# Kernel tuning notes

Measured on AMD Instinct MI355X. Metric: run time of the kernel, lower is better.

## Reference

```python
import jax, jax.numpy as jnp
import numpy as np
import math

B, SEQ_IN, D_IN = 4, 1028, 64
D = 1024          # hidden_size
H = 16            # num_heads
HD = D // H       # head_dim
L = 4             # num_layers
D_OUT = 1
EPS = 1e-6


def setup_inputs() -> dict:
    key = jax.random.key(0)
    ks = iter(jax.random.split(key, 32))
    s = 0.02
    inp = {}
    inp['x'] = jax.random.normal(next(ks), (B, SEQ_IN, D_IN), jnp.float32)
    # conv frontend (torch Conv1d weight layout: [out_ch, in_ch, k])
    inp['conv1_w'] = jax.random.normal(next(ks), (D // 2, D_IN, 3), jnp.float32) * s
    inp['conv1_b'] = jnp.zeros((D // 2,), jnp.float32)
    inp['conv2_w'] = jax.random.normal(next(ks), (D, D // 2, 3), jnp.float32) * s
    inp['conv2_b'] = jnp.zeros((D,), jnp.float32)
    # stacked per-layer params [L, ...]
    inp['lnA_w'] = jnp.ones((L, D), jnp.float32)
    inp['lnA_b'] = jnp.zeros((L, D), jnp.float32)
    inp['q_w'] = jax.random.normal(next(ks), (L, D, D), jnp.float32) * s
    inp['q_b'] = jnp.zeros((L, D), jnp.float32)
    inp['k_w'] = jax.random.normal(next(ks), (L, D, D), jnp.float32) * s
    inp['k_b'] = jnp.zeros((L, D), jnp.float32)
    inp['v_w'] = jax.random.normal(next(ks), (L, D, D), jnp.float32) * s
    inp['v_b'] = jnp.zeros((L, D), jnp.float32)
    inp['o_w'] = jax.random.normal(next(ks), (L, D, D), jnp.float32) * s
    inp['o_b'] = jnp.zeros((L, D), jnp.float32)
    inp['lnB_w'] = jnp.ones((L, D), jnp.float32)
    inp['lnB_b'] = jnp.zeros((L, D), jnp.float32)
    inp['f1_w'] = jax.random.normal(next(ks), (L, 2 * D, D), jnp.float32) * s
    inp['f1_b'] = jnp.zeros((L, 2 * D), jnp.float32)
    inp['f2_w'] = jax.random.normal(next(ks), (L, D, 2 * D), jnp.float32) * s
    inp['f2_b'] = jnp.zeros((L, D), jnp.float32)
    inp['fc_w'] = jax.random.normal(next(ks), (D_OUT, D), jnp.float32) * s
    inp['fc_b'] = jnp.zeros((D_OUT,), jnp.float32)
    return inp


def _layernorm(x, w, b):
    # torch-style: unbiased std (ddof=1), eps added to std (not var)
    mean = jnp.mean(x, axis=-1, keepdims=True)
    var = jnp.sum((x - mean) ** 2, axis=-1, keepdims=True) / (x.shape[-1] - 1)
    return w * ((x - mean) / (jnp.sqrt(var) + EPS)) + b


def _pos_encoding(S, d):
    pos = jnp.arange(S, dtype=jnp.float32)[:, None]
    div = jnp.exp(jnp.arange(0, d, 2, dtype=jnp.float32) * (-math.log(10000.0) / d))
    pe = jnp.zeros((S, d), jnp.float32)
    pe = pe.at[:, 0::2].set(jnp.sin(pos * div))
    pe = pe.at[:, 1::2].set(jnp.cos(pos * div))
    return pe


def _forward(x, conv1_w, conv1_b, conv2_w, conv2_b,
             lnA_w, lnA_b, q_w, q_b, k_w, k_b, v_w, v_b, o_w, o_b,
             lnB_w, lnB_b, f1_w, f1_b, f2_w, f2_b, fc_w, fc_b):
    dn = ('NCH', 'OIH', 'NCH')
    h = jnp.transpose(x, (0, 2, 1))                       # [B, D_in, S_in]
    h = jax.lax.conv_general_dilated(h, conv1_w, (1,), 'VALID', dimension_numbers=dn) + conv1_b[None, :, None]
    h = jax.lax.conv_general_dilated(h, conv2_w, (1,), 'VALID', dimension_numbers=dn) + conv2_b[None, :, None]
    h = jnp.transpose(h, (0, 2, 1))                       # [B, S, D]
    S = h.shape[1]
    h = h + _pos_encoding(S, D)[None]
    scale = 1.0 / math.sqrt(HD)

    def layer(xc, p):
        (lnaw, lnab, qw, qb, kw, kb, vw, vb, ow, ob,
         lnbw, lnbb, f1w, f1b, f2w, f2b) = p
        hn = _layernorm(xc, lnaw, lnab)
        q = (hn @ qw.T + qb).reshape(B, S, H, HD).transpose(0, 2, 1, 3)
        k = (hn @ kw.T + kb).reshape(B, S, H, HD).transpose(0, 2, 1, 3)
        v = (hn @ vw.T + vb).reshape(B, S, H, HD).transpose(0, 2, 1, 3)
        scores = jnp.einsum('bhsd,bhtd->bhst', q, k) * scale
        attn = scores / (1.0 + jnp.abs(scores))           # softsign, NOT softmax
        wv = jnp.einsum('bhst,bhtd->bhsd', attn, v)
        wv = wv.transpose(0, 2, 1, 3).reshape(B, S, D)
        xc = xc + (wv @ ow.T + ob)
        hn2 = _layernorm(xc, lnbw, lnbb)
        ff = jax.nn.relu(hn2 @ f1w.T + f1b) @ f2w.T + f2b
        return xc + ff, None

    params = (lnA_w, lnA_b, q_w, q_b, k_w, k_b, v_w, v_b, o_w, o_b,
              lnB_w, lnB_b, f1_w, f1_b, f2_w, f2_b)
    h, _ = jax.lax.scan(layer, h, params)
    pooled = jnp.mean(h, axis=1)                          # [B, D]
    return pooled @ fc_w.T + fc_b                         # [B, D_OUT]


def reference(x, conv1_w, conv1_b, conv2_w, conv2_b,
              lnA_w, lnA_b, q_w, q_b, k_w, k_b, v_w, v_b, o_w, o_b,
              lnB_w, lnB_b, f1_w, f1_b, f2_w, f2_b, fc_w, fc_b):
    return _forward(x, conv1_w, conv1_b, conv2_w, conv2_b,
                    lnA_w, lnA_b, q_w, q_b, k_w, k_b, v_w, v_b, o_w, o_b,
                    lnB_w, lnB_b, f1_w, f1_b, f2_w, f2_b, fc_w, fc_b)
```

## Files before the change

kernel.cpp:

```cpp
#include <hip/hip_runtime.h>
#include <hip/hip_bf16.h>
#include <math.h>

typedef __bf16 v8bf __attribute__((ext_vector_type(8)));
typedef float  v4f  __attribute__((ext_vector_type(4)));
typedef unsigned short v8us __attribute__((ext_vector_type(8)));

__device__ __forceinline__ unsigned short f2bfu(float f) {
    unsigned u = __builtin_bit_cast(unsigned, f);
    unsigned r = (u + 0x7fffu + ((u >> 16) & 1u)) >> 16;
    return (unsigned short)r;
}
__device__ __forceinline__ float bf2f(unsigned short u) {
    unsigned x = ((unsigned)u) << 16;
    return __builtin_bit_cast(float, x);
}

__device__ __forceinline__ long long swidx(int r, int k, int kt ) {
    return ((long long)((r >> 4) * kt + (k >> 5)) << 9)
         + (((k >> 3) & 3) << 7) + ((r & 15) << 3) + (k & 7);
}

#define GLDS16(g, s)                                                        \
    __builtin_amdgcn_global_load_lds(                                       \
        (const __attribute__((address_space(1))) void*)(g),                 \
        (__attribute__((address_space(3))) void*)(s), 16, 0, 0)

#define LOAD_CHUNK(R, C) do {                                               \
    const long long o_ = (long long)(C) << 9;                               \
    _Pragma("unroll")                                                       \
    for (int i_ = 0; i_ < 4; i_++) Ab[R][i_] = *(const v8bf*)(pa[i_] + o_); \
    _Pragma("unroll")                                                       \
    for (int j_ = 0; j_ < 4; j_++) Bb[R][j_] = *(const v8bf*)(pb[j_] + o_); \
} while (0)

#define MFMA_CHUNK(R) do {                                                  \
    _Pragma("unroll")                                                       \
    for (int i_ = 0; i_ < 4; i_++)                                          \
    _Pragma("unroll")                                                       \
    for (int j_ = 0; j_ < 4; j_++)                                          \
        acc[i_][j_] = __builtin_amdgcn_mfma_f32_16x16x32_bf16(              \
            Ab[R][i_], Bb[R][j_], acc[i_][j_], 0, 0, 0);                    \
} while (0)

__global__ __launch_bounds__(64, 2) void gemm_sw_k(
    const unsigned short* __restrict__ Asw,
    const unsigned short* __restrict__ Bsw,
    const float* __restrict__ bias,
    const float* __restrict__ res,
    float* __restrict__ Cf,
    unsigned short* __restrict__ Cb,
    unsigned short* __restrict__ Csw,
    unsigned short* __restrict__ Ct, int ctcol0,
    int M, int N, int K, int ldC, int relu)
{
    const int l = threadIdx.x;

    int bx = blockIdx.x, by = blockIdx.y;
    {
        int nbx = gridDim.x, nby = gridDim.y;
        if (((nbx & 7) == 0) && ((nby & 15) == 0)) {
            int bid   = by * nbx + bx;
            int xcd   = bid & 7;
            int local = bid >> 3;
            int rby = nby >> 2;
            int rbx = nbx >> 1;
            int u   = local & 15;
            int mt  = local >> 4;
            int mtxc = rbx >> 2;
            int mty = mt / mtxc;
            int mtx = mt - mty * mtxc;
            by = (xcd >> 1) * rby + (mty << 2) + (u >> 2);
            bx = (xcd & 1) * rbx + (mtx << 2) + (u & 3);
        } else {
            int nb = nbx * nby;
            if ((nb & 7) == 0) {
                int bid = by * nbx + bx;
                int nid = (bid & 7) * (nb >> 3) + (bid >> 3);
                by = nid / nbx;
                bx = nid - by * nbx;
            }
        }
    }
    const int m0 = by * 64;
    const int n0 = bx * 64;
    const int r16 = l & 15;
    const int qb  = l >> 4;
    const int kt = K >> 5;

    const unsigned short* pa[4];
#pragma unroll
    for (int i = 0; i < 4; i++)
        pa[i] = Asw + ((long long)(((m0 >> 4) + i) * kt) << 9) + l * 8;
    const unsigned short* pb[4];
#pragma unroll
    for (int j = 0; j < 4; j++)
        pb[j] = Bsw + ((long long)(((n0 >> 4) + j) * kt) << 9) + l * 8;

    v4f acc[4][4];
#pragma unroll
    for (int i = 0; i < 4; i++)
#pragma unroll
        for (int j = 0; j < 4; j++) acc[i][j] = (v4f){0.f, 0.f, 0.f, 0.f};

    v8bf Ab[4][4], Bb[4][4];

    LOAD_CHUNK(0, 0);
    LOAD_CHUNK(1, 1);
    LOAD_CHUNK(2, 2);

    int s = 0;
    for (; s < kt - 4; s += 4) {
        LOAD_CHUNK(3, s + 3); MFMA_CHUNK(0);
        LOAD_CHUNK(0, s + 4); MFMA_CHUNK(1);
        LOAD_CHUNK(1, s + 5); MFMA_CHUNK(2);
        LOAD_CHUNK(2, s + 6); MFMA_CHUNK(3);
    }
    LOAD_CHUNK(3, kt - 1);
    MFMA_CHUNK(0); MFMA_CHUNK(1); MFMA_CHUNK(2); MFMA_CHUNK(3);

    float bv[4];
#pragma unroll
    for (int j = 0; j < 4; j++) bv[j] = bias[n0 + 16 * j + r16];
    const int colbase = n0 + r16;
    const int nt = N >> 5;
#pragma unroll
    for (int i = 0; i < 4; i++) {
        int rowb = m0 + 16 * i + qb * 4;
#pragma unroll
        for (int j = 0; j < 4; j++) {
            int col = colbase + 16 * j;
            float v[4];
#pragma unroll
            for (int r = 0; r < 4; r++) v[r] = acc[i][j][r] + bv[j];
            if (Ct && col >= ctcol0) {
                ushort4 o;
                o.x = f2bfu(v[0]); o.y = f2bfu(v[1]);
                o.z = f2bfu(v[2]); o.w = f2bfu(v[3]);
                *(ushort4*)(Ct + ((long long)(rowb >> 10) << 20)
                            + (long long)(col - ctcol0) * 1024 + (rowb & 1023)) = o;
            } else if (Csw) {
#pragma unroll
                for (int r = 0; r < 4; r++) {
                    int row = rowb + r;
                    float vv = v[r];
                    if (relu) vv = fmaxf(vv, 0.f);
                    Csw[swidx(row, col, nt)] = f2bfu(vv);
                }
            } else {
#pragma unroll
                for (int r = 0; r < 4; r++) {
                    int row = rowb + r;
                    long long off = (long long)row * ldC + col;
                    float vv = v[r];
                    if (res)  vv += res[off];
                    if (relu) vv = fmaxf(vv, 0.f);
                    if (Cf) Cf[off] = vv;
                    if (Cb) ((unsigned short*)Cb)[off] = f2bfu(vv);
                }
            }
        }
    }
}

__global__ __launch_bounds__(256) void gemm_mfma_k(
    const __hip_bfloat16* __restrict__ A, int rpbA, long long bstrideA, int ldA,
    const __hip_bfloat16* __restrict__ B,
    const float* __restrict__ bias,
    const float* __restrict__ res,
    float* __restrict__ Cf,
    __hip_bfloat16* __restrict__ Cb,
    int M, int N, int K, int ldC, int relu)
{
    __shared__ __align__(16) __hip_bfloat16 As[2][8][64][8];
    __shared__ __align__(16) __hip_bfloat16 Bs[2][4][64][8];
    const int t  = threadIdx.x;
    const int w  = t >> 6;
    const int l  = t & 63;
    const int m0 = blockIdx.y * 128;
    const int n0 = blockIdx.x * 64;
    const int r16 = l & 15;
    const int qb  = l >> 4;
    const int wm = w >> 1, wn = w & 1;

    const __hip_bfloat16* gA[2];
#pragma unroll
    for (int tt = 0; tt < 2; tt++) {
        int arow = m0 + 16 * (2 * w + tt) + r16;
        gA[tt] = A + (long long)(arow / rpbA) * bstrideA
                   + (long long)(arow % rpbA) * ldA + qb * 8;
    }
    const __hip_bfloat16* gB = B + (long long)(n0 + 16 * w + r16) * K + qb * 8;

    v4f acc[4][2];
#pragma unroll
    for (int i = 0; i < 4; i++)
#pragma unroll
        for (int j = 0; j < 2; j++) acc[i][j] = (v4f){0.f, 0.f, 0.f, 0.f};

    GLDS16(gA[0], &As[0][2 * w + 0][0][0]);
    GLDS16(gA[1], &As[0][2 * w + 1][0][0]);
    GLDS16(gB,    &Bs[0][w][0][0]);
    __syncthreads();

    int cur = 0;
    for (int k0 = 32; k0 < K; k0 += 32) {
        v8bf af[4], bfr[2];
#pragma unroll
        for (int i = 0; i < 4; i++) af[i]  = *(const v8bf*)(&As[cur][4 * wm + i][l][0]);
#pragma unroll
        for (int j = 0; j < 2; j++) bfr[j] = *(const v8bf*)(&Bs[cur][2 * wn + j][l][0]);
        GLDS16(gA[0] + k0, &As[cur ^ 1][2 * w + 0][0][0]);
        GLDS16(gA[1] + k0, &As[cur ^ 1][2 * w + 1][0][0]);
        GLDS16(gB + k0,    &Bs[cur ^ 1][w][0][0]);
#pragma unroll
        for (int i = 0; i < 4; i++)
#pragma unroll
            for (int j = 0; j < 2; j++)
                acc[i][j] = __builtin_amdgcn_mfma_f32_16x16x32_bf16(
                    af[i], bfr[j], acc[i][j], 0, 0, 0);
        __syncthreads();
        cur ^= 1;
    }
    {
        v8bf af[4], bfr[2];
#pragma unroll
        for (int i = 0; i < 4; i++) af[i]  = *(const v8bf*)(&As[cur][4 * wm + i][l][0]);
#pragma unroll
        for (int j = 0; j < 2; j++) bfr[j] = *(const v8bf*)(&Bs[cur][2 * wn + j][l][0]);
#pragma unroll
        for (int i = 0; i < 4; i++)
#pragma unroll
            for (int j = 0; j < 2; j++)
                acc[i][j] = __builtin_amdgcn_mfma_f32_16x16x32_bf16(
                    af[i], bfr[j], acc[i][j], 0, 0, 0);
    }

    float bv[2];
#pragma unroll
    for (int j = 0; j < 2; j++) bv[j] = bias[n0 + 32 * wn + 16 * j + r16];
    const int colbase = n0 + 32 * wn + r16;
#pragma unroll
    for (int i = 0; i < 4; i++) {
        int rowb = m0 + 64 * wm + 16 * i + qb * 4;
#pragma unroll
        for (int j = 0; j < 2; j++) {
            int col = colbase + 16 * j;
#pragma unroll
            for (int r = 0; r < 4; r++) {
                int row = rowb + r;
                if (row >= M) continue;
                long long off = (long long)row * ldC + col;
                float vv = acc[i][j][r] + bv[j];
                if (res)  vv += res[off];
                if (relu) vv = fmaxf(vv, 0.f);
                if (Cf) Cf[off] = vv;
                if (Cb) ((unsigned short*)Cb)[off] = f2bfu(vv);
            }
        }
    }
}

__global__ __launch_bounds__(256) void attn_mfma_k(
    const unsigned short* __restrict__ QKV,
    const unsigned short* __restrict__ Vt,
    unsigned short* __restrict__ Osw)
{
    __shared__ __align__(16) unsigned short lds[25600];
    const int t = threadIdx.x, w = t >> 6, l = t & 63;
    const int bh = blockIdx.y, b = bh >> 4, h = bh & 15;
    const int s0 = blockIdx.x << 7;
    const int r16 = l & 15, q4 = l >> 4;
    const long long qrow0 = (long long)(b << 10) + s0;
    const int hoff = h << 6;

#pragma unroll
    for (int mi = 0; mi < 2; mi++)
#pragma unroll
        for (int kk = 0; kk < 2; kk++) {
            const unsigned short* g = QKV + (qrow0 + 32 * w + 16 * mi + r16) * 3072
                                      + hoff + 32 * kk + q4 * 8;
            GLDS16(g, &lds[(w * 4 + mi * 2 + kk) * 512]);
        }
    __syncthreads();
    v8bf qf[2][2];
#pragma unroll
    for (int mi = 0; mi < 2; mi++)
#pragma unroll
        for (int kk = 0; kk < 2; kk++)
            qf[mi][kk] = *(const v8bf*)&lds[(w * 4 + mi * 2 + kk) * 512 + l * 8];

    v4f oacc[2][4];
#pragma unroll
    for (int i = 0; i < 2; i++)
#pragma unroll
        for (int j = 0; j < 4; j++) oacc[i][j] = (v4f){0.f, 0.f, 0.f, 0.f};

    for (int t0 = 0; t0 < 1024; t0 += 64) {
#pragma unroll
        for (int rr = 0; rr < 2; rr++) {
            int r = 2 * w + rr, kk = r >> 2, j = r & 3;
            const unsigned short* gk = QKV
                + ((long long)(b << 10) + t0 + 16 * j + r16) * 3072
                + 1024 + hoff + 32 * kk + q4 * 8;
            GLDS16(gk, &lds[8192 + r * 512]);
            const unsigned short* gv = Vt + ((long long)b << 20)
                + (long long)(hoff + 16 * j + r16) * 1024 + t0 + 32 * kk + q4 * 8;
            GLDS16(gv, &lds[12288 + r * 512]);
        }
        __syncthreads();

        v8bf kf[2][4];
#pragma unroll
        for (int kk = 0; kk < 2; kk++)
#pragma unroll
            for (int j = 0; j < 4; j++)
                kf[kk][j] = *(const v8bf*)&lds[8192 + (kk * 4 + j) * 512 + l * 8];
        v4f sc[2][4];
#pragma unroll
        for (int i = 0; i < 2; i++)
#pragma unroll
            for (int j = 0; j < 4; j++) sc[i][j] = (v4f){0.f, 0.f, 0.f, 0.f};
#pragma unroll
        for (int kk = 0; kk < 2; kk++)
#pragma unroll
            for (int mi = 0; mi < 2; mi++)
#pragma unroll
                for (int j = 0; j < 4; j++)
                    sc[mi][j] = __builtin_amdgcn_mfma_f32_16x16x32_bf16(
                        qf[mi][kk], kf[kk][j], sc[mi][j], 0, 0, 0);

#pragma unroll
        for (int mi = 0; mi < 2; mi++)
#pragma unroll
            for (int j = 0; j < 4; j++)
#pragma unroll
                for (int r = 0; r < 4; r++) {
                    float v = sc[mi][j][r] * 0.125f;
                    float p = v * __builtin_amdgcn_rcpf(1.0f + fabsf(v));
                    lds[16384 + (32 * w + 16 * mi + q4 * 4 + r) * 72 + 16 * j + r16] = f2bfu(p);
                }

        v8bf pf[2][2], vf[2][4];
#pragma unroll
        for (int mi = 0; mi < 2; mi++)
#pragma unroll
            for (int kk = 0; kk < 2; kk++)
                pf[mi][kk] = *(const v8bf*)&lds[16384 + (32 * w + 16 * mi + r16) * 72
                                                + 32 * kk + q4 * 8];
#pragma unroll
        for (int kk = 0; kk < 2; kk++)
#pragma unroll
            for (int j = 0; j < 4; j++)
                vf[kk][j] = *(const v8bf*)&lds[12288 + (kk * 4 + j) * 512 + l * 8];
#pragma unroll
        for (int kk = 0; kk < 2; kk++)
#pragma unroll
            for (int mi = 0; mi < 2; mi++)
#pragma unroll
                for (int j = 0; j < 4; j++)
                    oacc[mi][j] = __builtin_amdgcn_mfma_f32_16x16x32_bf16(
                        pf[mi][kk], vf[kk][j], oacc[mi][j], 0, 0, 0);
        __syncthreads();
    }

#pragma unroll
    for (int mi = 0; mi < 2; mi++)
#pragma unroll
        for (int j = 0; j < 4; j++)
#pragma unroll
            for (int r = 0; r < 4; r++)
                lds[(32 * w + 16 * mi + q4 * 4 + r) * 72 + 16 * j + r16] =
                    f2bfu(oacc[mi][j][r]);
    __syncthreads();
    {
        int row = t >> 1, ch = (t & 1) << 5;
        int grow = (int)qrow0 + row;
#pragma unroll
        for (int i = 0; i < 4; i++) {
            int c0 = hoff + ch + 8 * i;
            v8us vv = *(const v8us*)&lds[row * 72 + ch + 8 * i];
            *(v8us*)(Osw + swidx(grow, c0, 32)) = vv;
        }
    }
}

__global__ __launch_bounds__(256) void layernorm_k(
    const float* __restrict__ x, const float* __restrict__ w,
    const float* __restrict__ b, unsigned short* __restrict__ ysw)
{
    int row = blockIdx.x;
    int t = threadIdx.x;
    float4 v = ((const float4*)(x + ((long long)row << 10)))[t];
    float s = v.x + v.y + v.z + v.w;
#pragma unroll
    for (int o = 32; o; o >>= 1) s += __shfl_down(s, o);
    __shared__ float red[4];
    __shared__ float red2[4];
    int wid = t >> 6, lane = t & 63;
    if (lane == 0) red[wid] = s;
    __syncthreads();
    float mean = (red[0] + red[1] + red[2] + red[3]) * (1.0f / 1024.0f);
    float dx = v.x - mean, dy = v.y - mean, dz = v.z - mean, dw = v.w - mean;
    float sq = dx * dx + dy * dy + dz * dz + dw * dw;
#pragma unroll
    for (int o = 32; o; o >>= 1) sq += __shfl_down(sq, o);
    if (lane == 0) red2[wid] = sq;
    __syncthreads();
    float var = (red2[0] + red2[1] + red2[2] + red2[3]) * (1.0f / 1023.0f);
    float inv = 1.0f / (sqrtf(var) + 1e-6f);
    float4 W  = ((const float4*)w)[t];
    float4 Bv = ((const float4*)b)[t];
    ushort4 o;
    o.x = f2bfu(W.x * (dx * inv) + Bv.x);
    o.y = f2bfu(W.y * (dy * inv) + Bv.y);
    o.z = f2bfu(W.z * (dz * inv) + Bv.z);
    o.w = f2bfu(W.w * (dw * inv) + Bv.w);
    int c0 = t << 2;
    *(ushort4*)(ysw + swidx(row, c0, 32)) = o;
}

__global__ __launch_bounds__(256) void add_pos_k(float* __restrict__ h)
{
    int idx = blockIdx.x * 256 + threadIdx.x;
    int d = idx & 1023;
    int s = (idx >> 10) & 1023;
    int e = d & ~1;
    float div = expf(-9.210340371976184f * (float)e * (1.0f / 1024.0f));
    float arg = (float)s * div;
    float pe = (d & 1) ? cosf(arg) : sinf(arg);
    h[idx] += pe;
}

__global__ __launch_bounds__(256) void convert_k(
    const float* __restrict__ src, unsigned short* __restrict__ dst, int n4)
{
    int i = blockIdx.x * 256 + threadIdx.x;
    if (i >= n4) return;
    float4 v = ((const float4*)src)[i];
    ushort4 o;
    o.x = f2bfu(v.x); o.y = f2bfu(v.y); o.z = f2bfu(v.z); o.w = f2bfu(v.w);
    ((ushort4*)dst)[i] = o;
}

__global__ __launch_bounds__(256) void convert_layer_sw_k(
    const float* __restrict__ q, const float* __restrict__ k,
    const float* __restrict__ v, const float* __restrict__ o,
    const float* __restrict__ f1, const float* __restrict__ f2,
    unsigned short* __restrict__ dst)
{
    int idx = blockIdx.x * 256 + threadIdx.x;
    const float* src;
    unsigned short* db;
    int Ksh, rf;
    if (idx < 0x100000) {
        int region = idx >> 18;
        rf = idx & 0x3FFFF;
        src = (region == 0) ? q : (region == 1) ? k : (region == 2) ? v : o;
        db = dst + ((long long)region << 20);
        Ksh = 10;
    } else if (idx < 0x180000) {
        rf = idx - 0x100000; src = f1; db = dst + (4LL << 20); Ksh = 10;
    } else {
        rf = idx - 0x180000; src = f2; db = dst + (6LL << 20); Ksh = 11;
    }
    float4 vv = ((const float4*)src)[rf];
    int flatf = rf << 2;
    int n  = flatf >> Ksh;
    int k0 = flatf & ((1 << Ksh) - 1);
    ushort4 ov;
    ov.x = f2bfu(vv.x); ov.y = f2bfu(vv.y); ov.z = f2bfu(vv.z); ov.w = f2bfu(vv.w);
    *(ushort4*)(db + swidx(n, k0, 1 << (Ksh - 5))) = ov;
}

__global__ __launch_bounds__(256) void concat3_k(
    const float* __restrict__ a, const float* __restrict__ b,
    const float* __restrict__ c, float* __restrict__ o)
{
    int i = blockIdx.x * 256 + threadIdx.x;
    o[i] = (i < 1024) ? a[i] : ((i < 2048) ? b[i - 1024] : c[i - 2048]);
}

__global__ __launch_bounds__(256) void reorder_w_k(
    const float* __restrict__ src, unsigned short* __restrict__ dst, int OC, int IC)
{
    int idx = blockIdx.x * 256 + threadIdx.x;
    if (idx >= OC * IC * 3) return;
    int k  = idx % 3;
    int ic = (idx / 3) % IC;
    int oc = idx / (3 * IC);
    dst[(oc * 3 + k) * IC + ic] = f2bfu(src[idx]);
}

__global__ __launch_bounds__(256) void meanpool_part_k(
    const float* __restrict__ h, float* __restrict__ part)
{
    int g = blockIdx.x;
    int b = g >> 6, rblk = g & 63;
    const float4* base = (const float4*)(h + ((long long)b << 20)
                                           + ((long long)(rblk * 16) << 10));
    float4 s = {0.f, 0.f, 0.f, 0.f};
#pragma unroll
    for (int i = 0; i < 16; i++) {
        float4 v = base[i * 256 + threadIdx.x];
        s.x += v.x; s.y += v.y; s.z += v.z; s.w += v.w;
    }
    ((float4*)part)[g * 256 + threadIdx.x] = s;
}

__global__ __launch_bounds__(256) void meanpool_red_k(
    const float* __restrict__ part, float* __restrict__ pooled)
{
    int idx = blockIdx.x * 256 + threadIdx.x;
    int b = idx >> 10, d = idx & 1023;
    const float* p = part + ((long long)(b * 64) << 10) + d;
    float s = 0.f;
#pragma unroll 8
    for (int r = 0; r < 64; r++) s += p[r << 10];
    pooled[idx] = s * (1.0f / 1024.0f);
}

__global__ __launch_bounds__(256) void fc_k(
    const float* __restrict__ p, const float* __restrict__ w,
    const float* __restrict__ fb, float* __restrict__ out)
{
    int b = blockIdx.x, t = threadIdx.x;
    float s = 0.f;
    for (int i = t; i < 1024; i += 256) s += p[(b << 10) + i] * w[i];
#pragma unroll
    for (int o = 32; o; o >>= 1) s += __shfl_down(s, o);
    __shared__ float red[4];
    if ((t & 63) == 0) red[t >> 6] = s;
    __syncthreads();
    if (t == 0) out[b] = red[0] + red[1] + red[2] + red[3] + fb[0];
}

extern "C" void kernel_launch(void* const* d_in, const int* in_sizes, int n_in,
                              void* d_out, int out_size, void* d_ws, size_t ws_size,
                              hipStream_t stream)
{
    const float* x    = (const float*)d_in[0];
    const float* c1w  = (const float*)d_in[1];
    const float* c1b  = (const float*)d_in[2];
    const float* c2w  = (const float*)d_in[3];
    const float* c2b  = (const float*)d_in[4];
    const float* lnAw = (const float*)d_in[5];
    const float* lnAb = (const float*)d_in[6];
    const float* qw   = (const float*)d_in[7];
    const float* qbi  = (const float*)d_in[8];
    const float* kw   = (const float*)d_in[9];
    const float* kbi  = (const float*)d_in[10];
    const float* vw   = (const float*)d_in[11];
    const float* vbi  = (const float*)d_in[12];
    const float* ow   = (const float*)d_in[13];
    const float* obi  = (const float*)d_in[14];
    const float* lnBw = (const float*)d_in[15];
    const float* lnBb = (const float*)d_in[16];
    const float* f1w  = (const float*)d_in[17];
    const float* f1b  = (const float*)d_in[18];
    const float* f2w  = (const float*)d_in[19];
    const float* f2b  = (const float*)d_in[20];
    const float* fcw  = (const float*)d_in[21];
    const float* fcb  = (const float*)d_in[22];
    float* out = (float*)d_out;

    float* ws = (float*)d_ws;
    typedef __hip_bfloat16 bf;
    typedef unsigned short us;
    float* h    = ws;
    us* hn_b    = (us*)(ws + 4194304);
    us* qkv_b   = (us*)(ws + 6291456);
    us* ff_b    = qkv_b;
    us* wq_b    = (us*)(ws + 12582912);
    us* wo_b    = (us*)(ws + 14155776);
    us* wf1_b   = (us*)(ws + 14680064);
    us* wf2_b   = (us*)(ws + 15728640);
    us* xb      = (us*)(ws + 16777216);
    us* h1b     = (us*)(ws + 16912896);
    us* w1t_b   = (us*)(ws + 17963520);
    us* w2t_b   = (us*)(ws + 18012672);
    float* pooled = ws + 18799104;
    us* Vt      = (us*)(ws + 18803200);
    float* bqkv = ws + 20900352;
    float* mp_part = ws + 20903424;

    convert_k<<<dim3(257), 256, 0, stream>>>(x, xb, 65792);
    reorder_w_k<<<dim3(384),  256, 0, stream>>>(c1w, w1t_b, 512, 64);
    reorder_w_k<<<dim3(6144), 256, 0, stream>>>(c2w, w2t_b, 1024, 512);

    gemm_mfma_k<<<dim3(8, 33), 256, 0, stream>>>(
        (const bf*)xb, 1026, 1028LL * 64, 64, (const bf*)w1t_b,
        c1b, nullptr, nullptr, (bf*)h1b, 4104, 512, 192, 512, 0);
    gemm_mfma_k<<<dim3(16, 32), 256, 0, stream>>>(
        (const bf*)h1b, 1024, 1026LL * 512, 512, (const bf*)w2t_b,
        c2b, nullptr, h, nullptr, 4096, 1024, 1536, 1024, 0);
    add_pos_k<<<dim3(16384), 256, 0, stream>>>(h);

    for (int l = 0; l < 4; l++) {
        long long wo  = (long long)l * 1048576;
        long long wo2 = (long long)l * 2097152;
        convert_layer_sw_k<<<dim3(8192), 256, 0, stream>>>(
            qw + wo, kw + wo, vw + wo, ow + wo, f1w + wo2, f2w + wo2, wq_b);
        concat3_k<<<dim3(12), 256, 0, stream>>>(qbi + l * 1024, kbi + l * 1024,
                                                vbi + l * 1024, bqkv);

        layernorm_k<<<dim3(4096), 256, 0, stream>>>(h, lnAw + l * 1024, lnAb + l * 1024, hn_b);
        gemm_sw_k<<<dim3(48, 64), 64, 0, stream>>>(
            hn_b, wq_b, bqkv, nullptr, nullptr, qkv_b, nullptr, Vt, 2048,
            4096, 3072, 1024, 3072, 0);
        attn_mfma_k<<<dim3(8, 64), 256, 0, stream>>>(qkv_b, Vt, hn_b);
        gemm_sw_k<<<dim3(16, 64), 64, 0, stream>>>(
            hn_b, wo_b, obi + l * 1024, h, h, nullptr, nullptr, nullptr, 0,
            4096, 1024, 1024, 1024, 0);
        layernorm_k<<<dim3(4096), 256, 0, stream>>>(h, lnBw + l * 1024, lnBb + l * 1024, hn_b);
        gemm_sw_k<<<dim3(32, 64), 64, 0, stream>>>(
            hn_b, wf1_b, f1b + l * 2048, nullptr, nullptr, nullptr, ff_b, nullptr, 0,
            4096, 2048, 1024, 2048, 1);
        gemm_sw_k<<<dim3(16, 64), 64, 0, stream>>>(
            ff_b, wf2_b, f2b + l * 1024, h, h, nullptr, nullptr, nullptr, 0,
            4096, 1024, 2048, 1024, 0);
    }

    meanpool_part_k<<<dim3(256), 256, 0, stream>>>(h, mp_part);
    meanpool_red_k<<<dim3(16), 256, 0, stream>>>(mp_part, pooled);
    fc_k<<<dim3(4), 256, 0, stream>>>(pooled, fcw, fcb, out);
}
```

Measured before the change: 1.122 ms.

## Double-buffer K/V tiles in attention and use two-wave GEMM blocks

The attention kernel now prefetches the next 64-key K/V tile into a second LDS buffer while the current tile is processed. This moves the P scratch to the start of LDS and drops the per-iteration load-then-sync stall. The swizzled GEMM switches to 128-thread blocks, each wave computing an adjacent 64-column tile, so grids halve in x and the A rows are shared across two waves. Grid swizzle conditions change with the new grid sizes, and LDS layout offsets must not overlap the P scratch.

```diff
diff --git a/kernel.cpp b/kernel.cpp
--- a/kernel.cpp
+++ b/kernel.cpp
@@ -43,7 +43,7 @@
             Ab[R][i_], Bb[R][j_], acc[i_][j_], 0, 0, 0);                    \
 } while (0)
 
-__global__ __launch_bounds__(64, 2) void gemm_sw_k(
+__global__ __launch_bounds__(128, 2) void gemm_sw_k(
     const unsigned short* __restrict__ Asw,
     const unsigned short* __restrict__ Bsw,
     const float* __restrict__ bias,
@@ -54,7 +54,8 @@
     unsigned short* __restrict__ Ct, int ctcol0,
     int M, int N, int K, int ldC, int relu)
 {
-    const int l = threadIdx.x;
+    const int wv = threadIdx.x >> 6;
+    const int l  = threadIdx.x & 63;
 
     int bx = blockIdx.x, by = blockIdx.y;
     {
@@ -83,7 +84,7 @@
         }
     }
     const int m0 = by * 64;
-    const int n0 = bx * 64;
+    const int n0 = bx * 128 + wv * 64;
     const int r16 = l & 15;
     const int qb  = l >> 4;
     const int kt = K >> 5;
@@ -274,6 +275,21 @@
     const long long qrow0 = (long long)(b << 10) + s0;
     const int hoff = h << 6;
 
+#define LOAD_KV(T0, KVW) do {                                               \
+    _Pragma("unroll")                                                       \
+    for (int rr_ = 0; rr_ < 2; rr_++) {                                     \
+        int r_ = 2 * w + rr_, kk_ = r_ >> 2, j_ = r_ & 3;                   \
+        const unsigned short* gk_ = QKV                                     \
+            + ((long long)(b << 10) + (T0) + 16 * j_ + r16) * 3072          \
+            + 1024 + hoff + 32 * kk_ + q4 * 8;                              \
+        GLDS16(gk_, &lds[(KVW) + r_ * 512]);                                \
+        const unsigned short* gv_ = Vt + ((long long)b << 20)               \
+            + (long long)(hoff + 16 * j_ + r16) * 1024 + (T0)               \
+            + 32 * kk_ + q4 * 8;                                            \
+        GLDS16(gv_, &lds[(KVW) + 4096 + r_ * 512]);                         \
+    }                                                                       \
+} while (0)
+
 #pragma unroll
     for (int mi = 0; mi < 2; mi++)
 #pragma unroll
@@ -282,6 +298,7 @@
                                       + hoff + 32 * kk + q4 * 8;
             GLDS16(g, &lds[(w * 4 + mi * 2 + kk) * 512]);
         }
+    LOAD_KV(0, 9216);
     __syncthreads();
     v8bf qf[2][2];
 #pragma unroll
@@ -289,6 +306,7 @@
 #pragma unroll
         for (int kk = 0; kk < 2; kk++)
             qf[mi][kk] = *(const v8bf*)&lds[(w * 4 + mi * 2 + kk) * 512 + l * 8];
+    __syncthreads();
 
     v4f oacc[2][4];
 #pragma unroll
@@ -296,26 +314,17 @@
 #pragma unroll
         for (int j = 0; j < 4; j++) oacc[i][j] = (v4f){0.f, 0.f, 0.f, 0.f};
 
-    for (int t0 = 0; t0 < 1024; t0 += 64) {
-#pragma unroll
-        for (int rr = 0; rr < 2; rr++) {
-            int r = 2 * w + rr, kk = r >> 2, j = r & 3;
-            const unsigned short* gk = QKV
-                + ((long long)(b << 10) + t0 + 16 * j + r16) * 3072
-                + 1024 + hoff + 32 * kk + q4 * 8;
-            GLDS16(gk, &lds[8192 + r * 512]);
-            const unsigned short* gv = Vt + ((long long)b << 20)
-                + (long long)(hoff + 16 * j + r16) * 1024 + t0 + 32 * kk + q4 * 8;
-            GLDS16(gv, &lds[12288 + r * 512]);
-        }
-        __syncthreads();
+    int cur = 0;
+    for (int it = 0; it < 16; ++it) {
+        const int kvr = 9216 + cur * 8192;
+        if (it < 15) LOAD_KV((it + 1) * 64, 9216 + (cur ^ 1) * 8192);
 
         v8bf kf[2][4];
 #pragma unroll
         for (int kk = 0; kk < 2; kk++)
 #pragma unroll
             for (int j = 0; j < 4; j++)
-                kf[kk][j] = *(const v8bf*)&lds[8192 + (kk * 4 + j) * 512 + l * 8];
+                kf[kk][j] = *(const v8bf*)&lds[kvr + (kk * 4 + j) * 512 + l * 8];
         v4f sc[2][4];
 #pragma unroll
         for (int i = 0; i < 2; i++)
@@ -338,7 +347,7 @@
                 for (int r = 0; r < 4; r++) {
                     float v = sc[mi][j][r] * 0.125f;
                     float p = v * __builtin_amdgcn_rcpf(1.0f + fabsf(v));
-                    lds[16384 + (32 * w + 16 * mi + q4 * 4 + r) * 72 + 16 * j + r16] = f2bfu(p);
+                    lds[(32 * w + 16 * mi + q4 * 4 + r) * 72 + 16 * j + r16] = f2bfu(p);
                 }
 
         v8bf pf[2][2], vf[2][4];
@@ -346,13 +355,13 @@
         for (int mi = 0; mi < 2; mi++)
 #pragma unroll
             for (int kk = 0; kk < 2; kk++)
-                pf[mi][kk] = *(const v8bf*)&lds[16384 + (32 * w + 16 * mi + r16) * 72
+                pf[mi][kk] = *(const v8bf*)&lds[(32 * w + 16 * mi + r16) * 72
                                                 + 32 * kk + q4 * 8];
 #pragma unroll
         for (int kk = 0; kk < 2; kk++)
 #pragma unroll
             for (int j = 0; j < 4; j++)
-                vf[kk][j] = *(const v8bf*)&lds[12288 + (kk * 4 + j) * 512 + l * 8];
+                vf[kk][j] = *(const v8bf*)&lds[kvr + 4096 + (kk * 4 + j) * 512 + l * 8];
 #pragma unroll
         for (int kk = 0; kk < 2; kk++)
 #pragma unroll
@@ -362,7 +371,9 @@
                     oacc[mi][j] = __builtin_amdgcn_mfma_f32_16x16x32_bf16(
                         pf[mi][kk], vf[kk][j], oacc[mi][j], 0, 0, 0);
         __syncthreads();
-    }
+        cur ^= 1;
+    }
+#undef LOAD_KV
 
 #pragma unroll
     for (int mi = 0; mi < 2; mi++)
@@ -605,18 +616,18 @@
                                                 vbi + l * 1024, bqkv);
 
         layernorm_k<<<dim3(4096), 256, 0, stream>>>(h, lnAw + l * 1024, lnAb + l * 1024, hn_b);
-        gemm_sw_k<<<dim3(48, 64), 64, 0, stream>>>(
+        gemm_sw_k<<<dim3(24, 64), 128, 0, stream>>>(
             hn_b, wq_b, bqkv, nullptr, nullptr, qkv_b, nullptr, Vt, 2048,
             4096, 3072, 1024, 3072, 0);
         attn_mfma_k<<<dim3(8, 64), 256, 0, stream>>>(qkv_b, Vt, hn_b);
-        gemm_sw_k<<<dim3(16, 64), 64, 0, stream>>>(
+        gemm_sw_k<<<dim3(8, 64), 128, 0, stream>>>(
             hn_b, wo_b, obi + l * 1024, h, h, nullptr, nullptr, nullptr, 0,
             4096, 1024, 1024, 1024, 0);
         layernorm_k<<<dim3(4096), 256, 0, stream>>>(h, lnBw + l * 1024, lnBb + l * 1024, hn_b);
-        gemm_sw_k<<<dim3(32, 64), 64, 0, stream>>>(
+        gemm_sw_k<<<dim3(16, 64), 128, 0, stream>>>(
             hn_b, wf1_b, f1b + l * 2048, nullptr, nullptr, nullptr, ff_b, nullptr, 0,
             4096, 2048, 1024, 2048, 1);
-        gemm_sw_k<<<dim3(16, 64), 64, 0, stream>>>(
+        gemm_sw_k<<<dim3(8, 64), 128, 0, stream>>>(
             ff_b, wf2_b, f2b + l * 1024, h, h, nullptr, nullptr, nullptr, 0,
             4096, 1024, 2048, 1024, 0);
     }
```

After: 1.110 ms. No clear change (-1.1%).
